# Kernel optimization log

Measured on AMD Instinct MI355X. Metric: run time of the kernel, lower is better.

## Reference

```python
import jax, jax.numpy as jnp
import numpy as np

SPACE_TOKEN = 63
STRIDE = 2
B, F, T, W = 16, 512, 8192, 4096


def setup_inputs() -> dict:
    key = jax.random.key(0)
    k1, k2, k3 = jax.random.split(key, 3)
    word_preds = jax.random.normal(k1, (B, F, W), dtype=jnp.float32)
    char_features = jax.random.normal(k2, (B, F, T), dtype=jnp.float32)
    target_chars = jax.random.randint(k3, (B, T), 0, 64, dtype=jnp.int32)
    return {"word_preds": word_preds, "char_features": char_features, "target_chars": target_chars}


def _per_batch(wp, cf, ch):
    # wp: (F, W) predicted word vectors; cf: (F, T) char features; ch: (T,) char ids
    Tn = ch.shape[0]
    Wn = wp.shape[1]
    space = ch == SPACE_TOKEN
    cum = jnp.cumsum(space.astype(jnp.int32))  # spaces seen up to and including t
    n_spaces = cum[-1]
    # span k lives strictly between space #k and space #(k+1) (0-indexed spaces).
    # a non-space char at t (with cum[t] spaces before it) belongs to span cum[t]-1.
    seg = jnp.where(space | (cum == 0), Tn, cum - 1)  # invalid chars -> dump segment Tn
    counts = jax.ops.segment_sum(jnp.ones((Tn,), jnp.int32), seg, num_segments=Tn + 1)[:Tn]
    sums = jax.ops.segment_sum(cf.T, seg, num_segments=Tn + 1)[:Tn]  # (Tn, F)
    # position of space #k via one-hot scatter of positions
    sid = jnp.where(space, cum - 1, Tn)
    pos_k = jax.ops.segment_sum(jnp.arange(Tn, dtype=jnp.int32), sid, num_segments=Tn + 1)[:Tn]
    word_pos = pos_k // STRIDE
    k = jnp.arange(Tn, dtype=jnp.int32)
    # valid span: a following space exists, span non-empty, word_pos in range
    valid = (k < n_spaces - 1) & (counts > 0) & (word_pos < Wn)
    target = sums / jnp.maximum(counts, 1).astype(sums.dtype)[:, None]  # span mean (detached in torch)
    target = jax.lax.stop_gradient(target)
    pred = wp[:, jnp.clip(word_pos, 0, Wn - 1)].T  # (Tn, F) gather of predictions
    mse = jnp.mean((pred - target) ** 2, axis=1)  # per-span mean over feat dim (F.mse_loss)
    return jnp.sum(jnp.where(valid, mse, 0.0)), jnp.sum(valid.astype(jnp.int32))


def reference(word_preds, char_features, target_chars):
    losses, cnts = jax.vmap(_per_batch)(word_preds, char_features, target_chars)
    total = jnp.sum(losses)
    count = jnp.sum(cnts)
    return jnp.where(count > 0, total / jnp.maximum(count, 1).astype(total.dtype), jnp.float32(0.0))
```

## Files before the change

kernel.cpp:

```cpp
#include <hip/hip_runtime.h>


constexpr int SPACE_TOKEN = 63;
constexpr int B = 16;
constexpr int FDIM = 512;
constexpr int T = 8192;
constexpr int W = 4096;

__global__ __launch_bounds__(1024) void k_find_spaces(
    const int* __restrict__ chars, int* __restrict__ spacePos,
    int* __restrict__ nspaces, int* __restrict__ validCount) {
  const int b = blockIdx.x;
  const int* c = chars + (size_t)b * T;
  int* pos = spacePos + (size_t)b * T;
  __shared__ int s_wtot[16];
  __shared__ int s_wpair[16];
  const int tid = threadIdx.x;
  const int lane = tid & 63;
  const int wid = tid >> 6;

  const int4* c4 = (const int4*)c;
  const int4 a0 = c4[tid * 2];
  const int4 a1 = c4[tid * 2 + 1];
  int v[8] = {a0.x, a0.y, a0.z, a0.w, a1.x, a1.y, a1.z, a1.w};
  int nxt = SPACE_TOKEN + 1;
  if (tid < 1023) nxt = c[tid * 8 + 8];

  int cnt = 0;
  int pairs = 0;
  #pragma unroll
  for (int i = 0; i < 8; ++i) cnt += (v[i] == SPACE_TOKEN);
  #pragma unroll
  for (int i = 0; i < 7; ++i)
    pairs += (v[i] == SPACE_TOKEN) && (v[i + 1] == SPACE_TOKEN);
  pairs += (v[7] == SPACE_TOKEN) && (nxt == SPACE_TOKEN);

  int inc = cnt;
  int pr = pairs;
  #pragma unroll
  for (int o = 1; o < 64; o <<= 1) {
    const int n = __shfl_up(inc, o);
    if (lane >= o) inc += n;
  }
  #pragma unroll
  for (int o = 32; o > 0; o >>= 1) pr += __shfl_down(pr, o);
  if (lane == 63) s_wtot[wid] = inc;
  if (lane == 0) s_wpair[wid] = pr;
  __syncthreads();
  int wexc = 0;
  for (int w = 0; w < wid; ++w) wexc += s_wtot[w];
  int base = wexc + inc - cnt;
  #pragma unroll
  for (int i = 0; i < 8; ++i)
    if (v[i] == SPACE_TOKEN) pos[base++] = tid * 8 + i;
  if (tid == 0) {
    int S = 0, P = 0;
    for (int w = 0; w < 16; ++w) { S += s_wtot[w]; P += s_wpair[w]; }
    nspaces[b] = S;
    validCount[b] = (S > 1 ? S - 1 : 0) - P;
  }
}

__device__ __forceinline__ int swz(int u) { return u ^ ((u >> 3) & 7); }

__global__ __launch_bounds__(256) void k_span_loss(
    const float* __restrict__ wp, const float* __restrict__ cf,
    const int* __restrict__ spacePos, const int* __restrict__ nspaces,
    float* __restrict__ partials) {
  const int idx = blockIdx.x;
  const int b = idx >> 9;
  __shared__ float rowf[T];
  __shared__ float csum[256];
  __shared__ float cexc[256];
  __shared__ float s_red[4];
  const int tid = threadIdx.x;
  const int lane = tid & 63;
  const int wid = tid >> 6;
  const float4* s4 = (const float4*)(cf + (size_t)idx * T);
  float4* r4 = (float4*)rowf;

  #pragma unroll
  for (int i = 0; i < 8; ++i) {
    const int u = i * 256 + tid;
    const float4* gsrc = s4 + swz(u);
    float4* ldst = r4 + (i * 256 + wid * 64);
    __builtin_amdgcn_global_load_lds(
        (const __attribute__((address_space(1))) void*)(const void*)gsrc,
        (__attribute__((address_space(3))) void*)(void*)ldst, 16, 0, 0);
  }

  const int* pos = spacePos + (size_t)b * T;
  const float* wrow = wp + (size_t)idx * W;
  const int S = nspaces[b];
  const int p0r = pos[tid];
  const int p1r = pos[tid + 1];
  const float wv = wrow[(p0r >> 1) & (W - 1)];

  __syncthreads();

  float4 v[8];
  #pragma unroll
  for (int i = 0; i < 8; ++i) v[i] = r4[swz(tid * 8 + i)];
  float run = 0.f;
  #pragma unroll
  for (int i = 0; i < 8; ++i) {
    v[i].x = (run += v[i].x);
    v[i].y = (run += v[i].y);
    v[i].z = (run += v[i].z);
    v[i].w = (run += v[i].w);
  }
  #pragma unroll
  for (int i = 0; i < 8; ++i) r4[swz(tid * 8 + i)] = v[i];
  csum[tid] = run;
  __syncthreads();

  if (tid < 64) {
    const float4 sv = ((const float4*)csum)[tid];
    const float l1 = sv.x + sv.y;
    const float l2 = l1 + sv.z;
    const float tot = l2 + sv.w;
    float inc = tot;
    #pragma unroll
    for (int o = 1; o < 64; o <<= 1) {
      const float n = __shfl_up(inc, o);
      if (tid >= o) inc += n;
    }
    const float exc = inc - tot;
    ((float4*)cexc)[tid] = make_float4(exc, exc + sv.x, exc + l1, exc + l2);
  }
  __syncthreads();

  float acc = 0.f;
  if (tid < S - 1) {
    const int cnt = p1r - p0r - 1;
    if (cnt > 0) {
      const int ta = p1r - 1;
      const float Pa = rowf[(swz(ta >> 2) << 2) | (ta & 3)] + cexc[ta >> 5];
      const float Pb = rowf[(swz(p0r >> 2) << 2) | (p0r & 3)] + cexc[p0r >> 5];
      const float mean = (Pa - Pb) / (float)cnt;
      const float d = wv - mean;
      acc += d * d;
    }
  }
  for (int k = tid + 256; k < S - 1; k += 256) {
    const int p0 = pos[k];
    const int p1 = pos[k + 1];
    const int cnt = p1 - p0 - 1;
    if (cnt > 0) {
      const int ta = p1 - 1;
      const float Pa = rowf[(swz(ta >> 2) << 2) | (ta & 3)] + cexc[ta >> 5];
      const float Pb = rowf[(swz(p0 >> 2) << 2) | (p0 & 3)] + cexc[p0 >> 5];
      const float mean = (Pa - Pb) / (float)cnt;
      const float d = wrow[p0 >> 1] - mean;
      acc += d * d;
    }
  }
  #pragma unroll
  for (int o = 32; o > 0; o >>= 1) acc += __shfl_down(acc, o);
  if (lane == 0) s_red[wid] = acc;
  __syncthreads();
  if (tid == 0) partials[idx] = s_red[0] + s_red[1] + s_red[2] + s_red[3];
}

__global__ __launch_bounds__(256) void k_finalize(
    const float* __restrict__ partials, const int* __restrict__ validCount,
    float* __restrict__ out) {
  __shared__ float s_red[4];
  __shared__ int s_cnt[4];
  const int tid = threadIdx.x;
  const int lane = tid & 63;
  const int wid = tid >> 6;
  float s = 0.f;
  for (int i = tid; i < B * FDIM; i += 256) s += partials[i];
  int cnt = 0;
  for (int i = tid; i < B; i += 256) cnt += validCount[i];
  for (int o = 32; o > 0; o >>= 1) {
    s += __shfl_down(s, o);
    cnt += __shfl_down(cnt, o);
  }
  if (lane == 0) { s_red[wid] = s; s_cnt[wid] = cnt; }
  __syncthreads();
  if (tid == 0) {
    const float total = s_red[0] + s_red[1] + s_red[2] + s_red[3];
    const int c = s_cnt[0] + s_cnt[1] + s_cnt[2] + s_cnt[3];
    out[0] = (c > 0) ? total / ((float)FDIM * (float)c) : 0.f;
  }
}

extern "C" void kernel_launch(void* const* d_in, const int* in_sizes, int n_in,
                              void* d_out, int out_size, void* d_ws, size_t ws_size,
                              hipStream_t stream) {
  const float* wp = (const float*)d_in[0];
  const float* cf = (const float*)d_in[1];
  const int* chars = (const int*)d_in[2];
  float* out = (float*)d_out;

  char* ws = (char*)d_ws;
  int* spacePos = (int*)ws;
  int* nspaces = (int*)(ws + (size_t)B * T * 4);
  int* validCount = nspaces + B;
  float* partials = (float*)(validCount + B);

  k_find_spaces<<<B, 1024, 0, stream>>>(chars, spacePos, nspaces, validCount);
  k_span_loss<<<B * FDIM, 256, 0, stream>>>(wp, cf, spacePos, nspaces, partials);
  k_finalize<<<1, 256, 0, stream>>>(partials, validCount, out);
}
```

Before: 74.57 us.

## Process eight feature rows per block with double-buffered async LDS staging

Each block now handles eight consecutive feature rows instead of one. While a row is being prefix-summed and scored, the next row is staged into a second LDS buffer with global_load_lds, using explicit vmcnt waits and raw barriers. The space positions and word-prediction gathers are loaded once per block and reused across the eight rows. This trades per-block launch and latency-exposure cost for fewer blocks (1024), doubled LDS use (64KB+) that lowers occupancy, and a serial loop inside each block.

After: 74.37 us. About the same (-0.3%).

```diff
diff --git a/kernel.cpp b/kernel.cpp
--- a/kernel.cpp
+++ b/kernel.cpp
@@ -6,6 +6,8 @@
 constexpr int FDIM = 512;
 constexpr int T = 8192;
 constexpr int W = 4096;
+constexpr int ROWS = 8;
+constexpr int NPART = B * FDIM / ROWS;
 
 __global__ __launch_bounds__(1024) void k_find_spaces(
     const int* __restrict__ chars, int* __restrict__ spacePos,
@@ -26,8 +28,7 @@
   int nxt = SPACE_TOKEN + 1;
   if (tid < 1023) nxt = c[tid * 8 + 8];
 
-  int cnt = 0;
-  int pairs = 0;
+  int cnt = 0, pairs = 0;
   #pragma unroll
   for (int i = 0; i < 8; ++i) cnt += (v[i] == SPACE_TOKEN);
   #pragma unroll
@@ -35,8 +36,7 @@
     pairs += (v[i] == SPACE_TOKEN) && (v[i + 1] == SPACE_TOKEN);
   pairs += (v[7] == SPACE_TOKEN) && (nxt == SPACE_TOKEN);
 
-  int inc = cnt;
-  int pr = pairs;
+  int inc = cnt, pr = pairs;
   #pragma unroll
   for (int o = 1; o < 64; o <<= 1) {
     const int n = __shfl_up(inc, o);
@@ -63,103 +63,129 @@
 
 __device__ __forceinline__ int swz(int u) { return u ^ ((u >> 3) & 7); }
 
+#define BAR_VM8() do { asm volatile("s_waitcnt vmcnt(8)" ::: "memory"); \
+  __builtin_amdgcn_s_barrier(); asm volatile("" ::: "memory"); } while (0)
+#define BAR_VM0() do { asm volatile("s_waitcnt vmcnt(0)" ::: "memory"); \
+  __builtin_amdgcn_s_barrier(); asm volatile("" ::: "memory"); } while (0)
+#define BAR_LGKM() do { asm volatile("s_waitcnt lgkmcnt(0)" ::: "memory"); \
+  __builtin_amdgcn_s_barrier(); asm volatile("" ::: "memory"); } while (0)
+
+__device__ __forceinline__ void stage_row(const float4* __restrict__ src,
+                                          float* dst, int tid, int wid) {
+  float4* d4 = (float4*)dst;
+  #pragma unroll
+  for (int i = 0; i < 8; ++i) {
+    const int u = i * 256 + tid;
+    const float4* gsrc = src + swz(u);
+    float4* ldst = d4 + (i * 256 + wid * 64);
+    __builtin_amdgcn_global_load_lds(
+        (const __attribute__((address_space(1))) void*)(const void*)gsrc,
+        (__attribute__((address_space(3))) void*)(void*)ldst, 16, 0, 0);
+  }
+}
+
 __global__ __launch_bounds__(256) void k_span_loss(
     const float* __restrict__ wp, const float* __restrict__ cf,
     const int* __restrict__ spacePos, const int* __restrict__ nspaces,
     float* __restrict__ partials) {
-  const int idx = blockIdx.x;
-  const int b = idx >> 9;
-  __shared__ float rowf[T];
-  __shared__ float csum[256];
-  __shared__ float cexc[256];
+  const int blk = blockIdx.x;
+  const int row0 = blk * ROWS;
+  const int b = row0 >> 9;
+  __shared__ alignas(16) float buf[2][T];
+  __shared__ alignas(16) float csum[256];
+  __shared__ alignas(16) float cexc[256];
   __shared__ float s_red[4];
   const int tid = threadIdx.x;
   const int lane = tid & 63;
   const int wid = tid >> 6;
-  const float4* s4 = (const float4*)(cf + (size_t)idx * T);
-  float4* r4 = (float4*)rowf;
-
-  #pragma unroll
-  for (int i = 0; i < 8; ++i) {
-    const int u = i * 256 + tid;
-    const float4* gsrc = s4 + swz(u);
-    float4* ldst = r4 + (i * 256 + wid * 64);
-    __builtin_amdgcn_global_load_lds(
-        (const __attribute__((address_space(1))) void*)(const void*)gsrc,
-        (__attribute__((address_space(3))) void*)(void*)ldst, 16, 0, 0);
-  }
+
+  stage_row((const float4*)(cf + (size_t)row0 * T), buf[0], tid, wid);
 
   const int* pos = spacePos + (size_t)b * T;
-  const float* wrow = wp + (size_t)idx * W;
   const int S = nspaces[b];
   const int p0r = pos[tid];
   const int p1r = pos[tid + 1];
-  const float wv = wrow[(p0r >> 1) & (W - 1)];
-
-  __syncthreads();
-
-  float4 v[8];
-  #pragma unroll
-  for (int i = 0; i < 8; ++i) v[i] = r4[swz(tid * 8 + i)];
-  float run = 0.f;
-  #pragma unroll
-  for (int i = 0; i < 8; ++i) {
-    v[i].x = (run += v[i].x);
-    v[i].y = (run += v[i].y);
-    v[i].z = (run += v[i].z);
-    v[i].w = (run += v[i].w);
-  }
-  #pragma unroll
-  for (int i = 0; i < 8; ++i) r4[swz(tid * 8 + i)] = v[i];
-  csum[tid] = run;
-  __syncthreads();
-
-  if (tid < 64) {
-    const float4 sv = ((const float4*)csum)[tid];
-    const float l1 = sv.x + sv.y;
-    const float l2 = l1 + sv.z;
-    const float tot = l2 + sv.w;
-    float inc = tot;
+  const int gidx = (p0r >> 1) & (W - 1);
+  float wv[ROWS];
+  #pragma unroll
+  for (int r = 0; r < ROWS; ++r)
+    wv[r] = wp[(size_t)(row0 + r) * W + gidx];
+
+  float acc = 0.f;
+  #pragma unroll 1
+  for (int r = 0; r < ROWS; ++r) {
+    if (r + 1 < ROWS)
+      stage_row((const float4*)(cf + (size_t)(row0 + r + 1) * T),
+                buf[(r + 1) & 1], tid, wid);
+    if (r + 1 < ROWS) { BAR_VM8(); } else { BAR_VM0(); }
+
+    float* rowf = buf[r & 1];
+    float4* r4 = (float4*)rowf;
+
+    float4 v[8];
     #pragma unroll
-    for (int o = 1; o < 64; o <<= 1) {
-      const float n = __shfl_up(inc, o);
-      if (tid >= o) inc += n;
-    }
-    const float exc = inc - tot;
-    ((float4*)cexc)[tid] = make_float4(exc, exc + sv.x, exc + l1, exc + l2);
-  }
-  __syncthreads();
-
-  float acc = 0.f;
-  if (tid < S - 1) {
-    const int cnt = p1r - p0r - 1;
-    if (cnt > 0) {
-      const int ta = p1r - 1;
-      const float Pa = rowf[(swz(ta >> 2) << 2) | (ta & 3)] + cexc[ta >> 5];
-      const float Pb = rowf[(swz(p0r >> 2) << 2) | (p0r & 3)] + cexc[p0r >> 5];
-      const float mean = (Pa - Pb) / (float)cnt;
-      const float d = wv - mean;
-      acc += d * d;
-    }
-  }
-  for (int k = tid + 256; k < S - 1; k += 256) {
-    const int p0 = pos[k];
-    const int p1 = pos[k + 1];
-    const int cnt = p1 - p0 - 1;
-    if (cnt > 0) {
-      const int ta = p1 - 1;
-      const float Pa = rowf[(swz(ta >> 2) << 2) | (ta & 3)] + cexc[ta >> 5];
-      const float Pb = rowf[(swz(p0 >> 2) << 2) | (p0 & 3)] + cexc[p0 >> 5];
-      const float mean = (Pa - Pb) / (float)cnt;
-      const float d = wrow[p0 >> 1] - mean;
-      acc += d * d;
-    }
-  }
+    for (int i = 0; i < 8; ++i) v[i] = r4[swz(tid * 8 + i)];
+    float run = 0.f;
+    #pragma unroll
+    for (int i = 0; i < 8; ++i) {
+      v[i].x = (run += v[i].x);
+      v[i].y = (run += v[i].y);
+      v[i].z = (run += v[i].z);
+      v[i].w = (run += v[i].w);
+    }
+    #pragma unroll
+    for (int i = 0; i < 8; ++i) r4[swz(tid * 8 + i)] = v[i];
+    csum[tid] = run;
+    BAR_LGKM();
+
+    if (tid < 64) {
+      const float4 sv = ((const float4*)csum)[tid];
+      const float l1 = sv.x + sv.y;
+      const float l2 = l1 + sv.z;
+      const float tot = l2 + sv.w;
+      float inc = tot;
+      #pragma unroll
+      for (int o = 1; o < 64; o <<= 1) {
+        const float n = __shfl_up(inc, o);
+        if (tid >= o) inc += n;
+      }
+      const float exc = inc - tot;
+      ((float4*)cexc)[tid] = make_float4(exc, exc + sv.x, exc + l1, exc + l2);
+    }
+    BAR_LGKM();
+
+    if (tid < S - 1) {
+      const int cnt = p1r - p0r - 1;
+      if (cnt > 0) {
+        const int ta = p1r - 1;
+        const float Pa = rowf[(swz(ta >> 2) << 2) | (ta & 3)] + cexc[ta >> 5];
+        const float Pb = rowf[(swz(p0r >> 2) << 2) | (p0r & 3)] + cexc[p0r >> 5];
+        const float mean = (Pa - Pb) / (float)cnt;
+        const float d = wv[r] - mean;
+        acc += d * d;
+      }
+    }
+    for (int k = tid + 256; k < S - 1; k += 256) {
+      const int p0 = pos[k];
+      const int p1 = pos[k + 1];
+      const int cnt = p1 - p0 - 1;
+      if (cnt > 0) {
+        const int ta = p1 - 1;
+        const float Pa = rowf[(swz(ta >> 2) << 2) | (ta & 3)] + cexc[ta >> 5];
+        const float Pb = rowf[(swz(p0 >> 2) << 2) | (p0 & 3)] + cexc[p0 >> 5];
+        const float mean = (Pa - Pb) / (float)cnt;
+        const float d = wp[(size_t)(row0 + r) * W + (p0 >> 1)] - mean;
+        acc += d * d;
+      }
+    }
+    BAR_LGKM();
+  }
+
   #pragma unroll
   for (int o = 32; o > 0; o >>= 1) acc += __shfl_down(acc, o);
   if (lane == 0) s_red[wid] = acc;
   __syncthreads();
-  if (tid == 0) partials[idx] = s_red[0] + s_red[1] + s_red[2] + s_red[3];
+  if (tid == 0) partials[blk] = s_red[0] + s_red[1] + s_red[2] + s_red[3];
 }
 
 __global__ __launch_bounds__(256) void k_finalize(
@@ -171,7 +197,7 @@
   const int lane = tid & 63;
   const int wid = tid >> 6;
   float s = 0.f;
-  for (int i = tid; i < B * FDIM; i += 256) s += partials[i];
+  for (int i = tid; i < NPART; i += 256) s += partials[i];
   int cnt = 0;
   for (int i = tid; i < B; i += 256) cnt += validCount[i];
   for (int o = 32; o > 0; o >>= 1) {
@@ -202,6 +228,6 @@
   float* partials = (float*)(validCount + B);
 
   k_find_spaces<<<B, 1024, 0, stream>>>(chars, spacePos, nspaces, validCount);
-  k_span_loss<<<B * FDIM, 256, 0, stream>>>(wp, cf, spacePos, nspaces, partials);
+  k_span_loss<<<NPART, 256, 0, stream>>>(wp, cf, spacePos, nspaces, partials);
   k_finalize<<<1, 256, 0, stream>>>(partials, validCount, out);
 }
```
